# Performance work log

Measured on AMD Instinct MI355X. Metric: run time of the kernel, lower is better.

The kernel has to match this reference:

```python
import jax, jax.numpy as jnp
import numpy as np

N_NODES = 50000


def gcn_conv(x, W, b, src, dst, n):
    """PyG GCNConv: add self-loops, sym-normalize, linear, scatter-add."""
    loop = jnp.arange(n, dtype=src.dtype)
    s = jnp.concatenate([src, loop])  # [E+N]
    d = jnp.concatenate([dst, loop])
    deg = jax.ops.segment_sum(jnp.ones_like(s, dtype=x.dtype), d, num_segments=n)
    dinv = jnp.where(deg > 0, jax.lax.rsqrt(deg), 0.0)  # deg^-1/2
    norm = dinv[s] * dinv[d]  # [E+N]
    h = x @ W  # [N, out] dense GEMM first (in >= out)
    msg = h[s] * norm[:, None]  # gather + scale
    out = jax.ops.segment_sum(msg, d, num_segments=n)  # scatter-add
    return out + b


def setup_inputs() -> dict:
    key = jax.random.key(0)
    k1, k2, k3, k4, k5, k6, k7, k8 = jax.random.split(key, 8)
    in_c, hid_c, out_c = 512, 128, 64
    n, e, l = N_NODES, 800000, 100000
    x = jax.random.normal(k1, (n, in_c), dtype=jnp.float32)
    edge_index = jax.random.randint(k2, (2, e), 0, n, dtype=jnp.int64)
    edge_label_index = jax.random.randint(k3, (2, l), 0, n, dtype=jnp.int64)
    # Glorot-ish init for weights, zeros for biases (PyG default bias=zeros)
    W1 = jax.random.normal(k4, (in_c, hid_c), dtype=jnp.float32) / np.sqrt(in_c)
    b1 = jnp.zeros((hid_c,), dtype=jnp.float32)
    W2 = jax.random.normal(k5, (hid_c, out_c), dtype=jnp.float32) / np.sqrt(hid_c)
    b2 = jnp.zeros((out_c,), dtype=jnp.float32)
    return {"x": x, "edge_index": edge_index, "edge_label_index": edge_label_index,
            "W1": W1, "b1": b1, "W2": W2, "b2": b2}


def reference(x, edge_index, edge_label_index, W1, b1, W2, b2):
    n = x.shape[0]
    src, dst = edge_index[0], edge_index[1]
    z = jax.nn.relu(gcn_conv(x, W1, b1, src, dst, n))
    z = gcn_conv(z, W2, b2, src, dst, n)
    es, ed = edge_label_index[0], edge_label_index[1]
    return jnp.sum(z[es] * z[ed], axis=-1).reshape(-1)
```

## Files before the change

kernel.cpp:

```cpp
#include <hip/hip_runtime.h>

#define IN_C  512
#define HID_C 128
#define OUT_C 64

using short8 = __attribute__((ext_vector_type(8))) short;
using floatx4 = __attribute__((ext_vector_type(4))) float;

__device__ inline unsigned short f2bf(float f) {
    unsigned u = __builtin_bit_cast(unsigned, f);
    u += 0x7FFFu + ((u >> 16) & 1u);
    return (unsigned short)(u >> 16);
}
__device__ inline float bf2f(unsigned short h) {
    unsigned u = ((unsigned)h) << 16;
    return __builtin_bit_cast(float, u);
}
__device__ inline unsigned short f2h(float f) {
    _Float16 h = (_Float16)f;
    return __builtin_bit_cast(unsigned short, h);
}
__device__ inline float h2f(unsigned v) {
    return (float)__builtin_bit_cast(_Float16, (unsigned short)v);
}

__global__ void k_zero_int(int* __restrict__ p, int n) {
    int i = blockIdx.x * blockDim.x + threadIdx.x;
    if (i < n) p[i] = 0;
}

__global__ void k_count(const int* __restrict__ dst, int* __restrict__ cnt, int e) {
    int i = blockIdx.x * blockDim.x + threadIdx.x;
    if (i < e) atomicAdd(&cnt[dst[i]], 1);
}

__global__ void k_blocksum_dinv(const int* __restrict__ cnt, int* __restrict__ bsum,
                                float* __restrict__ dinv, int n) {
    __shared__ int sdata[256];
    int t = threadIdx.x;
    int i = blockIdx.x * 256 + t;
    int c = (i < n) ? cnt[i] : 0;
    if (i < n) dinv[i] = rsqrtf(1.0f + (float)c);
    sdata[t] = c;
    __syncthreads();
    for (int s = 128; s > 0; s >>= 1) {
        if (t < s) sdata[t] += sdata[t + s];
        __syncthreads();
    }
    if (t == 0) bsum[blockIdx.x] = sdata[0];
}

__global__ void k_scanpartials(int* __restrict__ bsum, int nb) {
    __shared__ int sdata[256];
    int t = threadIdx.x;
    int orig = (t < nb) ? bsum[t] : 0;
    sdata[t] = orig;
    __syncthreads();
    for (int off = 1; off < 256; off <<= 1) {
        int v = (t >= off) ? sdata[t - off] : 0;
        __syncthreads();
        sdata[t] += v;
        __syncthreads();
    }
    if (t < nb) bsum[t] = sdata[t] - orig;
}

__global__ void k_scanfinal(const int* __restrict__ cnt, const int* __restrict__ bsum_ex,
                            int* __restrict__ row_ptr, int n, int e_total) {
    __shared__ int sdata[256];
    int t = threadIdx.x;
    int i = blockIdx.x * 256 + t;
    int orig = (i < n) ? cnt[i] : 0;
    sdata[t] = orig;
    __syncthreads();
    for (int off = 1; off < 256; off <<= 1) {
        int v = (t >= off) ? sdata[t - off] : 0;
        __syncthreads();
        sdata[t] += v;
        __syncthreads();
    }
    if (i < n) row_ptr[i] = sdata[t] - orig + bsum_ex[blockIdx.x];
    if (i == 0) row_ptr[n] = e_total;
}

__global__ void k_fill(const int* __restrict__ src, const int* __restrict__ dst,
                       const int* __restrict__ row_ptr, int* __restrict__ cnt,
                       int* __restrict__ col, int e) {
    int i = blockIdx.x * blockDim.x + threadIdx.x;
    if (i < e) {
        int d = dst[i];
        int pos = atomicSub(&cnt[d], 1) - 1;
        col[row_ptr[d] + pos] = src[i];
    }
}

__global__ void k_prep_w2(const float* __restrict__ W1, unsigned short* __restrict__ hi1,
                          unsigned short* __restrict__ lo1, const float* __restrict__ W2,
                          unsigned short* __restrict__ hi2, unsigned short* __restrict__ lo2) {
    int i = blockIdx.x * blockDim.x + threadIdx.x;
    if (i < IN_C * HID_C) {
        int k = i / HID_C, n = i % HID_C;
        float v = W1[i];
        unsigned short h = f2bf(v);
        hi1[(long)n * IN_C + k] = h;
        lo1[(long)n * IN_C + k] = f2bf(v - bf2f(h));
    } else if (i < IN_C * HID_C + HID_C * OUT_C) {
        int j = i - IN_C * HID_C;
        int k = j / OUT_C, n = j % OUT_C;
        float v = W2[j];
        unsigned short h = f2bf(v);
        hi2[(long)n * HID_C + k] = h;
        lo2[(long)n * HID_C + k] = f2bf(v - bf2f(h));
    }
}

template <int K, int NPW>
__global__ __launch_bounds__(256) void k_gemm_mfma(
    const float* __restrict__ A, const unsigned short* __restrict__ Bt_hi,
    const unsigned short* __restrict__ Bt_lo, const float* __restrict__ dinv,
    unsigned short* __restrict__ Hs, int M) {
    constexpr int N = 64 * NPW;
    constexpr int LDA = 72;
    constexpr int NT = K / 64;
    __shared__ __align__(16) unsigned short As_hi[2][64 * LDA];
    __shared__ __align__(16) unsigned short As_lo[2][64 * LDA];

    const int tid = threadIdx.x;
    const int w = tid >> 6;
    const int lane = tid & 63;
    const int m = lane & 15;
    const int quad = lane >> 4;
    const int m0 = blockIdx.x * 64;

    const int srow = tid >> 4;
    const int skk = (tid & 15) << 2;

    floatx4 acc[4][NPW];
#pragma unroll
    for (int mi = 0; mi < 4; ++mi)
#pragma unroll
        for (int ni = 0; ni < NPW; ++ni) acc[mi][ni] = (floatx4){0.f, 0.f, 0.f, 0.f};

    float4 pf[4];
#pragma unroll
    for (int i = 0; i < 4; ++i) {
        int gm = m0 + srow + 16 * i;
        pf[i] = make_float4(0.f, 0.f, 0.f, 0.f);
        if (gm < M) pf[i] = *(const float4*)&A[(long)gm * K + skk];
    }
#pragma unroll
    for (int i = 0; i < 4; ++i) {
        ushort4 h, l;
        h.x = f2bf(pf[i].x); l.x = f2bf(pf[i].x - bf2f(h.x));
        h.y = f2bf(pf[i].y); l.y = f2bf(pf[i].y - bf2f(h.y));
        h.z = f2bf(pf[i].z); l.z = f2bf(pf[i].z - bf2f(h.z));
        h.w = f2bf(pf[i].w); l.w = f2bf(pf[i].w - bf2f(h.w));
        int off = (srow + 16 * i) * LDA + skk;
        *(ushort4*)&As_hi[0][off] = h;
        *(ushort4*)&As_lo[0][off] = l;
    }

    for (int t = 0; t < NT; ++t) {
        __syncthreads();
        const int buf = t & 1;
        if (t + 1 < NT) {
#pragma unroll
            for (int i = 0; i < 4; ++i) {
                int gm = m0 + srow + 16 * i;
                pf[i] = make_float4(0.f, 0.f, 0.f, 0.f);
                if (gm < M) pf[i] = *(const float4*)&A[(long)gm * K + (t + 1) * 64 + skk];
            }
        }
#pragma unroll
        for (int s = 0; s < 2; ++s) {
            short8 ah[4], al[4];
#pragma unroll
            for (int mi = 0; mi < 4; ++mi) {
                int off = (mi * 16 + m) * LDA + s * 32 + quad * 8;
                ah[mi] = *(const short8*)&As_hi[buf][off];
                al[mi] = *(const short8*)&As_lo[buf][off];
            }
#pragma unroll
            for (int ni = 0; ni < NPW; ++ni) {
                int n = (w * NPW + ni) * 16 + m;
                long boff = (long)n * K + t * 64 + s * 32 + quad * 8;
                short8 bh = *(const short8*)&Bt_hi[boff];
                short8 bl = *(const short8*)&Bt_lo[boff];
#pragma unroll
                for (int mi = 0; mi < 4; ++mi) {
                    acc[mi][ni] = __builtin_amdgcn_mfma_f32_16x16x32_bf16(ah[mi], bh, acc[mi][ni], 0, 0, 0);
                    acc[mi][ni] = __builtin_amdgcn_mfma_f32_16x16x32_bf16(ah[mi], bl, acc[mi][ni], 0, 0, 0);
                    acc[mi][ni] = __builtin_amdgcn_mfma_f32_16x16x32_bf16(al[mi], bh, acc[mi][ni], 0, 0, 0);
                }
            }
        }
        if (t + 1 < NT) {
#pragma unroll
            for (int i = 0; i < 4; ++i) {
                ushort4 h, l;
                h.x = f2bf(pf[i].x); l.x = f2bf(pf[i].x - bf2f(h.x));
                h.y = f2bf(pf[i].y); l.y = f2bf(pf[i].y - bf2f(h.y));
                h.z = f2bf(pf[i].z); l.z = f2bf(pf[i].z - bf2f(h.z));
                h.w = f2bf(pf[i].w); l.w = f2bf(pf[i].w - bf2f(h.w));
                int off = (srow + 16 * i) * LDA + skk;
                *(ushort4*)&As_hi[buf ^ 1][off] = h;
                *(ushort4*)&As_lo[buf ^ 1][off] = l;
            }
        }
    }

#pragma unroll
    for (int mi = 0; mi < 4; ++mi) {
#pragma unroll
        for (int r = 0; r < 4; ++r) {
            int row = m0 + mi * 16 + quad * 4 + r;
            if (row < M) {
                float dv = dinv[row];
#pragma unroll
                for (int ni = 0; ni < NPW; ++ni) {
                    int n = (w * NPW + ni) * 16 + m;
                    Hs[(long)row * N + n] = f2h(acc[mi][ni][r] * dv);
                }
            }
        }
    }
}

__global__ __launch_bounds__(256) void k_agg1(
    const unsigned short* __restrict__ h, const int* __restrict__ row_ptr,
    const int* __restrict__ col, const float* __restrict__ dinv,
    const float* __restrict__ bias, float* __restrict__ z, int n) {
    int node = blockIdx.x * 4 + (threadIdx.x >> 6);
    node = __builtin_amdgcn_readfirstlane(node);
    if (node >= n) return;
    int lane = threadIdx.x & 63;
    int q = lane >> 4, li = lane & 15;
    const uint4* hp = (const uint4*)h;
    float acc[8] = {0.f, 0.f, 0.f, 0.f, 0.f, 0.f, 0.f, 0.f};
    auto addrow = [&](uint4 v) {
        acc[0] += h2f(v.x); acc[1] += h2f(v.x >> 16);
        acc[2] += h2f(v.y); acc[3] += h2f(v.y >> 16);
        acc[4] += h2f(v.z); acc[5] += h2f(v.z >> 16);
        acc[6] += h2f(v.w); acc[7] += h2f(v.w >> 16);
    };
    if (q == 0) addrow(hp[(long)node * 16 + li]);
    int rs = row_ptr[node], re = row_ptr[node + 1];
    int j = rs + q;
    for (; j + 12 < re; j += 16) {
        int s0 = col[j], s1 = col[j + 4], s2 = col[j + 8], s3 = col[j + 12];
        uint4 v0 = hp[(long)s0 * 16 + li];
        uint4 v1 = hp[(long)s1 * 16 + li];
        uint4 v2 = hp[(long)s2 * 16 + li];
        uint4 v3 = hp[(long)s3 * 16 + li];
        addrow(v0); addrow(v1); addrow(v2); addrow(v3);
    }
    for (; j < re; j += 4) addrow(hp[(long)col[j] * 16 + li]);
#pragma unroll
    for (int k = 0; k < 8; ++k) {
        acc[k] += __shfl_xor(acc[k], 16);
        acc[k] += __shfl_xor(acc[k], 32);
    }
    if (q == 0) {
        float dv = dinv[node];
        const float4* bp = (const float4*)bias;
        float4 b0 = bp[li * 2], b1 = bp[li * 2 + 1];
        float4 o0, o1;
        o0.x = fmaxf(fmaf(acc[0], dv, b0.x), 0.f);
        o0.y = fmaxf(fmaf(acc[1], dv, b0.y), 0.f);
        o0.z = fmaxf(fmaf(acc[2], dv, b0.z), 0.f);
        o0.w = fmaxf(fmaf(acc[3], dv, b0.w), 0.f);
        o1.x = fmaxf(fmaf(acc[4], dv, b1.x), 0.f);
        o1.y = fmaxf(fmaf(acc[5], dv, b1.y), 0.f);
        o1.z = fmaxf(fmaf(acc[6], dv, b1.z), 0.f);
        o1.w = fmaxf(fmaf(acc[7], dv, b1.w), 0.f);
        ((float4*)z)[(long)node * 32 + li * 2] = o0;
        ((float4*)z)[(long)node * 32 + li * 2 + 1] = o1;
    }
}

__global__ __launch_bounds__(256) void k_agg2(
    const unsigned short* __restrict__ h, const int* __restrict__ row_ptr,
    const int* __restrict__ col, const float* __restrict__ dinv,
    const float* __restrict__ bias, float* __restrict__ z, int n) {
    int node = blockIdx.x * 4 + (threadIdx.x >> 6);
    node = __builtin_amdgcn_readfirstlane(node);
    if (node >= n) return;
    int lane = threadIdx.x & 63;
    int q = lane >> 4, li = lane & 15;
    const uint2* hp = (const uint2*)h;
    float acc[4] = {0.f, 0.f, 0.f, 0.f};
    auto addrow = [&](uint2 v) {
        acc[0] += h2f(v.x); acc[1] += h2f(v.x >> 16);
        acc[2] += h2f(v.y); acc[3] += h2f(v.y >> 16);
    };
    if (q == 0) addrow(hp[(long)node * 16 + li]);
    int rs = row_ptr[node], re = row_ptr[node + 1];
    int j = rs + q;
    for (; j + 12 < re; j += 16) {
        int s0 = col[j], s1 = col[j + 4], s2 = col[j + 8], s3 = col[j + 12];
        uint2 v0 = hp[(long)s0 * 16 + li];
        uint2 v1 = hp[(long)s1 * 16 + li];
        uint2 v2 = hp[(long)s2 * 16 + li];
        uint2 v3 = hp[(long)s3 * 16 + li];
        addrow(v0); addrow(v1); addrow(v2); addrow(v3);
    }
    for (; j < re; j += 4) addrow(hp[(long)col[j] * 16 + li]);
#pragma unroll
    for (int k = 0; k < 4; ++k) {
        acc[k] += __shfl_xor(acc[k], 16);
        acc[k] += __shfl_xor(acc[k], 32);
    }
    if (q == 0) {
        float dv = dinv[node];
        float4 b = ((const float4*)bias)[li];
        float4 o;
        o.x = fmaf(acc[0], dv, b.x);
        o.y = fmaf(acc[1], dv, b.y);
        o.z = fmaf(acc[2], dv, b.z);
        o.w = fmaf(acc[3], dv, b.w);
        ((float4*)z)[(long)node * 16 + li] = o;
    }
}

__global__ void k_dot(const float* __restrict__ z2, const int* __restrict__ es,
                      const int* __restrict__ ed, float* __restrict__ out, int L) {
    int gid = blockIdx.x * blockDim.x + threadIdx.x;
    int wid = gid >> 6;
    int lane = threadIdx.x & 63;
    int q = lane >> 4, li = lane & 15;
    int e = wid * 4 + q;
    if (e >= L) return;
    int a = es[e], b = ed[e];
    const float4* zp = (const float4*)z2;
    float4 za = zp[(long)a * 16 + li];
    float4 zb = zp[(long)b * 16 + li];
    float v = za.x * zb.x + za.y * zb.y + za.z * zb.z + za.w * zb.w;
#pragma unroll
    for (int off = 8; off > 0; off >>= 1) v += __shfl_xor(v, off);
    if (li == 0) out[e] = v;
}

extern "C" void kernel_launch(void* const* d_in, const int* in_sizes, int n_in,
                              void* d_out, int out_size, void* d_ws, size_t ws_size,
                              hipStream_t stream) {
    const float* x = (const float*)d_in[0];
    const int* ei = (const int*)d_in[1];
    const int* eli = (const int*)d_in[2];
    const float* W1 = (const float*)d_in[3];
    const float* b1 = (const float*)d_in[4];
    const float* W2 = (const float*)d_in[5];
    const float* b2 = (const float*)d_in[6];
    float* out = (float*)d_out;

    const int N = in_sizes[0] / IN_C;
    const int E = in_sizes[1] / 2;
    const int L = in_sizes[2] / 2;
    const int* src = ei;
    const int* dst = ei + E;
    const int* es = eli;
    const int* ed = eli + L;

    const int Npad = (N + 63) & ~63;
    const int Epad = (E + 3) & ~3;

    int* cnt = (int*)d_ws;
    int* row_ptr = cnt + Npad;
    int* bsum = row_ptr + Npad + 64;
    int* col = bsum + 256;
    float* dinv = (float*)(col + Epad);
    unsigned short* h1s = (unsigned short*)(dinv + Npad);
    float* z1 = (float*)(h1s + (long)N * HID_C);
    unsigned short* h2s = h1s;
    float* z2 = z1 + (long)N * HID_C;
    unsigned short* wt1_hi = (unsigned short*)(z2 + (long)N * OUT_C);
    unsigned short* wt1_lo = wt1_hi + IN_C * HID_C;
    unsigned short* wt2_hi = wt1_lo + IN_C * HID_C;
    unsigned short* wt2_lo = wt2_hi + HID_C * OUT_C;

    const int TPB = 256;
    const int nb = (N + 255) / 256;

    const int PW = IN_C * HID_C + HID_C * OUT_C;
    k_prep_w2<<<(PW + TPB - 1) / TPB, TPB, 0, stream>>>(W1, wt1_hi, wt1_lo, W2, wt2_hi, wt2_lo);

    k_zero_int<<<(Npad + TPB - 1) / TPB, TPB, 0, stream>>>(cnt, Npad);
    k_count<<<(E + TPB - 1) / TPB, TPB, 0, stream>>>(dst, cnt, E);
    k_blocksum_dinv<<<nb, 256, 0, stream>>>(cnt, bsum, dinv, N);
    k_scanpartials<<<1, 256, 0, stream>>>(bsum, nb);
    k_scanfinal<<<nb, 256, 0, stream>>>(cnt, bsum, row_ptr, N, E);
    k_fill<<<(E + TPB - 1) / TPB, TPB, 0, stream>>>(src, dst, row_ptr, cnt, col, E);

    k_gemm_mfma<IN_C, 2><<<(N + 63) / 64, 256, 0, stream>>>(x, wt1_hi, wt1_lo, dinv, h1s, N);
    k_agg1<<<(N + 3) / 4, 256, 0, stream>>>(h1s, row_ptr, col, dinv, b1, z1, N);

    k_gemm_mfma<HID_C, 1><<<(N + 63) / 64, 256, 0, stream>>>(z1, wt2_hi, wt2_lo, dinv, h2s, N);
    k_agg2<<<(N + 3) / 4, 256, 0, stream>>>(h2s, row_ptr, col, dinv, b2, z2, N);

    k_dot<<<((long)((L + 3) / 4) * 64 + TPB - 1) / TPB, TPB, 0, stream>>>(z2, es, ed, out, L);
}
```

Baseline: 367.6 us.

## Store GEMM output in 32-column slabs and split aggregation by feature slab

The GEMM epilogue now writes H in a slab-major layout (groups of 32 fp16 columns, each slab contiguous over nodes). The aggregation kernels launch one block group per slab, with each slab holding 64 bytes per node, so the gathered working set per pass is smaller and more likely to stay cached. In exchange, the CSR indices and row pointers are re-read once per slab, and each gather moves only 4 bytes per lane, which means more memory instructions and more blocks.

```diff
diff --git a/kernel.cpp b/kernel.cpp
--- a/kernel.cpp
+++ b/kernel.cpp
@@ -219,7 +219,7 @@
 #pragma unroll
                 for (int ni = 0; ni < NPW; ++ni) {
                     int n = (w * NPW + ni) * 16 + m;
-                    Hs[(long)row * N + n] = f2h(acc[mi][ni][r] * dv);
+                    Hs[((long)(n >> 5) * M + row) * 32 + (n & 31)] = f2h(acc[mi][ni][r] * dv);
                 }
             }
         }
@@ -229,96 +229,88 @@
 __global__ __launch_bounds__(256) void k_agg1(
     const unsigned short* __restrict__ h, const int* __restrict__ row_ptr,
     const int* __restrict__ col, const float* __restrict__ dinv,
-    const float* __restrict__ bias, float* __restrict__ z, int n) {
-    int node = blockIdx.x * 4 + (threadIdx.x >> 6);
+    const float* __restrict__ bias, float* __restrict__ z, int n, int nb) {
+    int bid = blockIdx.x;
+    int s = bid / nb;
+    int node = (bid % nb) * 4 + (threadIdx.x >> 6);
     node = __builtin_amdgcn_readfirstlane(node);
     if (node >= n) return;
     int lane = threadIdx.x & 63;
     int q = lane >> 4, li = lane & 15;
-    const uint4* hp = (const uint4*)h;
-    float acc[8] = {0.f, 0.f, 0.f, 0.f, 0.f, 0.f, 0.f, 0.f};
-    auto addrow = [&](uint4 v) {
-        acc[0] += h2f(v.x); acc[1] += h2f(v.x >> 16);
-        acc[2] += h2f(v.y); acc[3] += h2f(v.y >> 16);
-        acc[4] += h2f(v.z); acc[5] += h2f(v.z >> 16);
-        acc[6] += h2f(v.w); acc[7] += h2f(v.w >> 16);
-    };
-    if (q == 0) addrow(hp[(long)node * 16 + li]);
+    const unsigned* hp = (const unsigned*)h + (long)s * n * 16;
+    float a0 = 0.f, a1 = 0.f;
+    if (q == 0) {
+        unsigned v = hp[(long)node * 16 + li];
+        a0 = h2f(v); a1 = h2f(v >> 16);
+    }
     int rs = row_ptr[node], re = row_ptr[node + 1];
     int j = rs + q;
     for (; j + 12 < re; j += 16) {
         int s0 = col[j], s1 = col[j + 4], s2 = col[j + 8], s3 = col[j + 12];
-        uint4 v0 = hp[(long)s0 * 16 + li];
-        uint4 v1 = hp[(long)s1 * 16 + li];
-        uint4 v2 = hp[(long)s2 * 16 + li];
-        uint4 v3 = hp[(long)s3 * 16 + li];
-        addrow(v0); addrow(v1); addrow(v2); addrow(v3);
-    }
-    for (; j < re; j += 4) addrow(hp[(long)col[j] * 16 + li]);
-#pragma unroll
-    for (int k = 0; k < 8; ++k) {
-        acc[k] += __shfl_xor(acc[k], 16);
-        acc[k] += __shfl_xor(acc[k], 32);
-    }
+        unsigned v0 = hp[(long)s0 * 16 + li];
+        unsigned v1 = hp[(long)s1 * 16 + li];
+        unsigned v2 = hp[(long)s2 * 16 + li];
+        unsigned v3 = hp[(long)s3 * 16 + li];
+        a0 += h2f(v0) + h2f(v1) + h2f(v2) + h2f(v3);
+        a1 += h2f(v0 >> 16) + h2f(v1 >> 16) + h2f(v2 >> 16) + h2f(v3 >> 16);
+    }
+    for (; j < re; j += 4) {
+        unsigned v = hp[(long)col[j] * 16 + li];
+        a0 += h2f(v); a1 += h2f(v >> 16);
+    }
+    a0 += __shfl_xor(a0, 16); a0 += __shfl_xor(a0, 32);
+    a1 += __shfl_xor(a1, 16); a1 += __shfl_xor(a1, 32);
     if (q == 0) {
         float dv = dinv[node];
-        const float4* bp = (const float4*)bias;
-        float4 b0 = bp[li * 2], b1 = bp[li * 2 + 1];
-        float4 o0, o1;
-        o0.x = fmaxf(fmaf(acc[0], dv, b0.x), 0.f);
-        o0.y = fmaxf(fmaf(acc[1], dv, b0.y), 0.f);
-        o0.z = fmaxf(fmaf(acc[2], dv, b0.z), 0.f);
-        o0.w = fmaxf(fmaf(acc[3], dv, b0.w), 0.f);
-        o1.x = fmaxf(fmaf(acc[4], dv, b1.x), 0.f);
-        o1.y = fmaxf(fmaf(acc[5], dv, b1.y), 0.f);
-        o1.z = fmaxf(fmaf(acc[6], dv, b1.z), 0.f);
-        o1.w = fmaxf(fmaf(acc[7], dv, b1.w), 0.f);
-        ((float4*)z)[(long)node * 32 + li * 2] = o0;
-        ((float4*)z)[(long)node * 32 + li * 2 + 1] = o1;
+        float2 b = ((const float2*)bias)[s * 16 + li];
+        float2 o;
+        o.x = fmaxf(fmaf(a0, dv, b.x), 0.f);
+        o.y = fmaxf(fmaf(a1, dv, b.y), 0.f);
+        ((float2*)z)[(long)node * 64 + s * 16 + li] = o;
     }
 }
 
 __global__ __launch_bounds__(256) void k_agg2(
     const unsigned short* __restrict__ h, const int* __restrict__ row_ptr,
     const int* __restrict__ col, const float* __restrict__ dinv,
-    const float* __restrict__ bias, float* __restrict__ z, int n) {
-    int node = blockIdx.x * 4 + (threadIdx.x >> 6);
+    const float* __restrict__ bias, float* __restrict__ z, int n, int nb) {
+    int bid = blockIdx.x;
+    int s = bid / nb;
+    int node = (bid % nb) * 4 + (threadIdx.x >> 6);
     node = __builtin_amdgcn_readfirstlane(node);
     if (node >= n) return;
     int lane = threadIdx.x & 63;
     int q = lane >> 4, li = lane & 15;
-    const uint2* hp = (const uint2*)h;
-    float acc[4] = {0.f, 0.f, 0.f, 0.f};
-    auto addrow = [&](uint2 v) {
-        acc[0] += h2f(v.x); acc[1] += h2f(v.x >> 16);
-        acc[2] += h2f(v.y); acc[3] += h2f(v.y >> 16);
-    };
-    if (q == 0) addrow(hp[(long)node * 16 + li]);
+    const unsigned* hp = (const unsigned*)h + (long)s * n * 16;
+    float a0 = 0.f, a1 = 0.f;
+    if (q == 0) {
+        unsigned v = hp[(long)node * 16 + li];
+        a0 = h2f(v); a1 = h2f(v >> 16);
+    }
     int rs = row_ptr[node], re = row_ptr[node + 1];
     int j = rs + q;
     for (; j + 12 < re; j += 16) {
         int s0 = col[j], s1 = col[j + 4], s2 = col[j + 8], s3 = col[j + 12];
-        uint2 v0 = hp[(long)s0 * 16 + li];
-        uint2 v1 = hp[(long)s1 * 16 + li];
-        uint2 v2 = hp[(long)s2 * 16 + li];
-        uint2 v3 = hp[(long)s3 * 16 + li];
-        addrow(v0); addrow(v1); addrow(v2); addrow(v3);
-    }
-    for (; j < re; j += 4) addrow(hp[(long)col[j] * 16 + li]);
-#pragma unroll
-    for (int k = 0; k < 4; ++k) {
-        acc[k] += __shfl_xor(acc[k], 16);
-        acc[k] += __shfl_xor(acc[k], 32);
-    }
+        unsigned v0 = hp[(long)s0 * 16 + li];
+        unsigned v1 = hp[(long)s1 * 16 + li];
+        unsigned v2 = hp[(long)s2 * 16 + li];
+        unsigned v3 = hp[(long)s3 * 16 + li];
+        a0 += h2f(v0) + h2f(v1) + h2f(v2) + h2f(v3);
+        a1 += h2f(v0 >> 16) + h2f(v1 >> 16) + h2f(v2 >> 16) + h2f(v3 >> 16);
+    }
+    for (; j < re; j += 4) {
+        unsigned v = hp[(long)col[j] * 16 + li];
+        a0 += h2f(v); a1 += h2f(v >> 16);
+    }
+    a0 += __shfl_xor(a0, 16); a0 += __shfl_xor(a0, 32);
+    a1 += __shfl_xor(a1, 16); a1 += __shfl_xor(a1, 32);
     if (q == 0) {
         float dv = dinv[node];
-        float4 b = ((const float4*)bias)[li];
-        float4 o;
-        o.x = fmaf(acc[0], dv, b.x);
-        o.y = fmaf(acc[1], dv, b.y);
-        o.z = fmaf(acc[2], dv, b.z);
-        o.w = fmaf(acc[3], dv, b.w);
-        ((float4*)z)[(long)node * 16 + li] = o;
+        float2 b = ((const float2*)bias)[s * 16 + li];
+        float2 o;
+        o.x = fmaf(a0, dv, b.x);
+        o.y = fmaf(a1, dv, b.y);
+        ((float2*)z)[(long)node * 32 + s * 16 + li] = o;
     }
 }
 
@@ -379,6 +371,7 @@
 
     const int TPB = 256;
     const int nb = (N + 255) / 256;
+    const int nb4 = (N + 3) / 4;
 
     const int PW = IN_C * HID_C + HID_C * OUT_C;
     k_prep_w2<<<(PW + TPB - 1) / TPB, TPB, 0, stream>>>(W1, wt1_hi, wt1_lo, W2, wt2_hi, wt2_lo);
@@ -391,10 +384,10 @@
     k_fill<<<(E + TPB - 1) / TPB, TPB, 0, stream>>>(src, dst, row_ptr, cnt, col, E);
 
     k_gemm_mfma<IN_C, 2><<<(N + 63) / 64, 256, 0, stream>>>(x, wt1_hi, wt1_lo, dinv, h1s, N);
-    k_agg1<<<(N + 3) / 4, 256, 0, stream>>>(h1s, row_ptr, col, dinv, b1, z1, N);
+    k_agg1<<<4 * nb4, 256, 0, stream>>>(h1s, row_ptr, col, dinv, b1, z1, N, nb4);
 
     k_gemm_mfma<HID_C, 1><<<(N + 63) / 64, 256, 0, stream>>>(z1, wt2_hi, wt2_lo, dinv, h2s, N);
-    k_agg2<<<(N + 3) / 4, 256, 0, stream>>>(h2s, row_ptr, col, dinv, b2, z2, N);
+    k_agg2<<<2 * nb4, 256, 0, stream>>>(h2s, row_ptr, col, dinv, b2, z2, N, nb4);
 
     k_dot<<<((long)((L + 3) / 4) * 64 + TPB - 1) / TPB, TPB, 0, stream>>>(z2, es, ed, out, L);
 }
```

Result: slower. 426.2 us (+15.9%).
